# Kernel optimization log

Measured on AMD Instinct MI355X. Metric: run time of the kernel, lower is better.

Reference implementation:

```python
import jax, jax.numpy as jnp
import numpy as np

H = 256

def setup_inputs() -> dict:
    key = jax.random.key(0)
    ks = jax.random.split(key, 9)
    s = 1.0 / np.sqrt(H)
    x = jax.random.normal(ks[0], (8, 2048, H), dtype=jnp.float32)
    Wq = jax.random.uniform(ks[1], (H, H), jnp.float32, -s, s)
    bq = jax.random.uniform(ks[2], (H,), jnp.float32, -s, s)
    Wk = jax.random.uniform(ks[3], (H, H), jnp.float32, -s, s)
    bk = jax.random.uniform(ks[4], (H,), jnp.float32, -s, s)
    Wv = jax.random.uniform(ks[5], (H, H), jnp.float32, -s, s)
    bv = jax.random.uniform(ks[6], (H,), jnp.float32, -s, s)
    Ww = jax.random.uniform(ks[7], (H, 1), jnp.float32, -s, s)
    bw = jax.random.uniform(ks[8], (1,), jnp.float32, -s, s)
    return {"x": x, "Wq": Wq, "bq": bq, "Wk": Wk, "bk": bk,
            "Wv": Wv, "bv": bv, "Ww": Ww, "bw": bw}

def reference(x, Wq, bq, Wk, bk, Wv, bv, Ww, bw):
    # x: (B, N, H) — cross-asset attention over N assets
    q = x @ Wq + bq
    k = x @ Wk + bk
    v = x @ Wv + bv
    scale = 1.0 / jnp.sqrt(jnp.asarray(q.shape[-1], q.dtype))
    beta = jnp.einsum('bnd,bmd->bnm', q, k) * scale  # (B, N, N)
    beta = jax.nn.softmax(beta, axis=-1)
    # original: sum(value[:,None] * beta[...,None], dim=2) == beta @ v
    out = jnp.einsum('bnm,bmd->bnd', beta, v)
    final_scores = (out @ Ww + bw)[..., 0]  # (B, N)
    return final_scores
```

## Files before the change

### kernel.cpp

```cpp
#include <hip/hip_runtime.h>

#define H 256
#define NB 2048
#define BATCH 8
#define NSPLIT 8
#define KSPAN (NB / NSPLIT)

typedef unsigned short u16;
using bf16x8 = __attribute__((ext_vector_type(8))) __bf16;
using f32x4  = __attribute__((ext_vector_type(4))) float;

typedef const __attribute__((address_space(1))) void gv_t;
typedef __attribute__((address_space(3))) void lv_t;

__device__ __forceinline__ void gl_lds16(const void* g, void* l) {
    __builtin_amdgcn_global_load_lds((gv_t*)g, (lv_t*)l, 16, 0, 0);
}

#define MFMA(a, b, c) __builtin_amdgcn_mfma_f32_16x16x32_bf16(a, b, c, 0, 0, 0)

__device__ __forceinline__ u16 f2bf(float f) {
    union { float f; unsigned u; } v; v.f = f;
    unsigned r = v.u + 0x7fffu + ((v.u >> 16) & 1u);
    return (u16)(r >> 16);
}

__global__ __launch_bounds__(256) void prep_kernel(
        const float* __restrict__ Wq, const float* __restrict__ Wk,
        const float* __restrict__ Wv, const float* __restrict__ Ww,
        const float* __restrict__ bq,
        u16* __restrict__ aT, float* __restrict__ wvw, float* __restrict__ kbv) {
    int f = blockIdx.x, t = threadIdx.x;
    __shared__ float wkf[H];
    __shared__ float redp[4], redr[4];
    float wkval = Wk[f * H + t];
    wkf[t] = wkval;
    float p = Wv[f * H + t] * Ww[t];
    float r = wkval * bq[t];
    __syncthreads();
    float s = 0.f;
    #pragma unroll 8
    for (int d = 0; d < H; ++d) s += Wq[t * H + d] * wkf[d];
    aT[f * H + t] = f2bf(s * 0.0625f);
    for (int o = 32; o; o >>= 1) { p += __shfl_xor(p, o); r += __shfl_xor(r, o); }
    int w = t >> 6, lane = t & 63;
    if (lane == 0) { redp[w] = p; redr[w] = r; }
    __syncthreads();
    if (t == 0) {
        wvw[f] = redp[0] + redp[1] + redp[2] + redp[3];
        kbv[f] = redr[0] + redr[1] + redr[2] + redr[3];
    }
}

__global__ __launch_bounds__(256) void cvtu_kernel(
        const float* __restrict__ x, const float* __restrict__ wvw,
        const float* __restrict__ kbv, const float* __restrict__ bv,
        const float* __restrict__ Ww,
        u16* __restrict__ xbf, float* __restrict__ ue, float* __restrict__ ee) {
    int lane = threadIdx.x & 63;
    int row  = blockIdx.x * 4 + (threadIdx.x >> 6);
    float4 xv = *(const float4*)(x + row * H + lane * 4);
    ushort4 o;
    o.x = f2bf(xv.x); o.y = f2bf(xv.y); o.z = f2bf(xv.z); o.w = f2bf(xv.w);
    *(ushort4*)(xbf + row * H + lane * 4) = o;
    float4 wv = *(const float4*)(wvw + lane * 4);
    float s = xv.x * wv.x + xv.y * wv.y + xv.z * wv.z + xv.w * wv.w;
    float4 kv = *(const float4*)(kbv + lane * 4);
    float d = xv.x * kv.x + xv.y * kv.y + xv.z * kv.z + xv.w * kv.w;
    float4 bvv = *(const float4*)(bv + lane * 4);
    float4 www = *(const float4*)(Ww + lane * 4);
    float c = bvv.x * www.x + bvv.y * www.y + bvv.z * www.z + bvv.w * www.w;
    for (int o2 = 32; o2; o2 >>= 1) {
        s += __shfl_xor(s, o2); d += __shfl_xor(d, o2); c += __shfl_xor(c, o2);
    }
    if (lane == 0) {
        float e = __expf(d * 0.0625f);
        ue[row] = e * (s + c);
        ee[row] = e;
    }
}

__global__ __launch_bounds__(256) void projT_kernel(
        const u16* __restrict__ xbf, const u16* __restrict__ aT,
        u16* __restrict__ T) {
    __shared__ u16 bt[16384];
    int tid = threadIdx.x;
    int mb = blockIdx.x * 128, nb = blockIdx.y * 64;
    int w = tid >> 6, lane = tid & 63;
    int l15 = lane & 15, quad = lane >> 4;

    {
        const u16* gsrc = aT + (nb + w * 16 + l15) * H + quad * 8;
        for (int ks = 0; ks < 8; ++ks)
            gl_lds16(gsrc + ks * 32, bt + (w * 8 + ks) * 512);
    }

    bf16x8 a[2][8];
    for (int mi = 0; mi < 2; ++mi) {
        const u16* abase = xbf + (mb + w * 32 + mi * 16 + l15) * H + quad * 8;
        for (int ks = 0; ks < 8; ++ks) a[mi][ks] = *(const bf16x8*)(abase + ks * 32);
    }
    __syncthreads();

    f32x4 acc[2][4] = {};
    for (int ks = 0; ks < 8; ++ks)
        for (int t = 0; t < 4; ++t) {
            bf16x8 b = *(const bf16x8*)(bt + ((t * 8 + ks) * 64 + lane) * 8);
            acc[0][t] = MFMA(a[0][ks], b, acc[0][t]);
            acc[1][t] = MFMA(a[1][ks], b, acc[1][t]);
        }

    for (int mi = 0; mi < 2; ++mi) {
        int m = mb + w * 32 + mi * 16 + quad * 4;
        for (int t = 0; t < 4; ++t) {
            int n = nb + t * 16 + l15;
            for (int r = 0; r < 4; ++r)
                T[(m + r) * H + n] = f2bf(acc[mi][t][r]);
        }
    }
}

__global__ __launch_bounds__(256, 4) void attn_kernel(
        const u16* __restrict__ T, const u16* __restrict__ xbf,
        const float* __restrict__ ue, const float* __restrict__ ee,
        float* __restrict__ pnum, float* __restrict__ pden) {
    __shared__ u16 kt[16384];
    __shared__ float utile[64], etile[64];
    int tid = threadIdx.x;
    int b = blockIdx.y, qb = blockIdx.x * 128, sp = blockIdx.z;
    int w = tid >> 6, lane = tid & 63, l15 = lane & 15, quad = lane >> 4;

    const u16* qb0 = T + (size_t)(b * NB + qb + w * 32 + l15) * H + quad * 8;
    float ls[2][4] = {}, as_[2][4] = {};

    const int kb0 = sp * KSPAN;
    #pragma unroll 1
    for (int kb = kb0; kb < kb0 + KSPAN; kb += 64) {
        const u16* ksrc = xbf + (size_t)(b * NB + kb) * H;
        {
            const u16* gsrc = ksrc + (w * 16 + l15) * H + quad * 8;
            for (int ks = 0; ks < 8; ++ks)
                gl_lds16(gsrc + ks * 32, kt + (w * 8 + ks) * 512);
        }
        if (tid < 64) utile[tid] = ue[b * NB + kb + tid];
        else if (tid < 128) etile[tid - 64] = ee[b * NB + kb + (tid - 64)];
        __syncthreads();

        f32x4 acc[2][4] = {};
        #pragma unroll 1
        for (int half = 0; half < 2; ++half) {
            bf16x8 aq[2][4];
            for (int mi = 0; mi < 2; ++mi)
                for (int kk = 0; kk < 4; ++kk)
                    aq[mi][kk] = *(const bf16x8*)(qb0 + mi * 16 * H + (half * 4 + kk) * 32);
            for (int kk = 0; kk < 4; ++kk) {
                int ks = half * 4 + kk;
                for (int t = 0; t < 4; ++t) {
                    bf16x8 bfr = *(const bf16x8*)(kt + ((t * 8 + ks) * 64 + lane) * 8);
                    acc[0][t] = MFMA(aq[0][kk], bfr, acc[0][t]);
                    acc[1][t] = MFMA(aq[1][kk], bfr, acc[1][t]);
                }
            }
        }

        float uv[4], ev[4];
        for (int t = 0; t < 4; ++t) { uv[t] = utile[t * 16 + l15]; ev[t] = etile[t * 16 + l15]; }

        for (int mi = 0; mi < 2; ++mi)
            for (int r = 0; r < 4; ++r) {
                float p0 = __expf(acc[mi][0][r]), p1 = __expf(acc[mi][1][r]);
                float p2 = __expf(acc[mi][2][r]), p3 = __expf(acc[mi][3][r]);
                ls[mi][r]  += (p0 * ev[0] + p1 * ev[1]) + (p2 * ev[2] + p3 * ev[3]);
                as_[mi][r] += (p0 * uv[0] + p1 * uv[1]) + (p2 * uv[2] + p3 * uv[3]);
            }
        __syncthreads();
    }

    for (int mi = 0; mi < 2; ++mi)
        for (int r = 0; r < 4; ++r)
            for (int o = 1; o < 16; o <<= 1) {
                ls[mi][r]  += __shfl_xor(ls[mi][r], o);
                as_[mi][r] += __shfl_xor(as_[mi][r], o);
            }

    if (l15 == 0) {
        for (int mi = 0; mi < 2; ++mi) {
            size_t base = (size_t)(sp * BATCH + b) * NB + qb + w * 32 + mi * 16 + quad * 4;
            for (int r = 0; r < 4; ++r) {
                pnum[base + r] = as_[mi][r];
                pden[base + r] = ls[mi][r];
            }
        }
    }
}

__global__ __launch_bounds__(256) void finalize_kernel(
        const float* __restrict__ pnum, const float* __restrict__ pden,
        const float* __restrict__ bw, float* __restrict__ out) {
    int i = blockIdx.x * 256 + threadIdx.x;
    float num = 0.f, den = 0.f;
    for (int sp = 0; sp < NSPLIT; ++sp) {
        num += pnum[sp * (BATCH * NB) + i];
        den += pden[sp * (BATCH * NB) + i];
    }
    out[i] = num / den + bw[0];
}

extern "C" void kernel_launch(void* const* d_in, const int* in_sizes, int n_in,
                              void* d_out, int out_size, void* d_ws, size_t ws_size,
                              hipStream_t stream) {
    (void)in_sizes; (void)n_in; (void)out_size; (void)ws_size;
    const float* x  = (const float*)d_in[0];
    const float* Wq = (const float*)d_in[1];
    const float* bq = (const float*)d_in[2];
    const float* Wk = (const float*)d_in[3];
    const float* bk = (const float*)d_in[4];  (void)bk;
    const float* Wv = (const float*)d_in[5];
    const float* bv = (const float*)d_in[6];
    const float* Ww = (const float*)d_in[7];
    const float* bw = (const float*)d_in[8];
    float* out = (float*)d_out;

    u16* xbf = (u16*)d_ws;
    u16* Tbf = xbf + 4194304;
    u16* aT  = Tbf + 4194304;
    float* wvw = (float*)(aT + 65536);
    float* kbv = wvw + 256;
    float* ue  = kbv + 256;
    float* ee  = ue + 16384;
    float* pnum = ee + 16384;
    float* pden = pnum + NSPLIT * BATCH * NB;

    hipLaunchKernelGGL(prep_kernel, dim3(256), dim3(256), 0, stream,
                       Wq, Wk, Wv, Ww, bq, aT, wvw, kbv);
    hipLaunchKernelGGL(cvtu_kernel, dim3(4096), dim3(256), 0, stream,
                       x, wvw, kbv, bv, Ww, xbf, ue, ee);
    hipLaunchKernelGGL(projT_kernel, dim3(128, 4), dim3(256), 0, stream,
                       xbf, aT, Tbf);
    hipLaunchKernelGGL(attn_kernel, dim3(16, 8, NSPLIT), dim3(256), 0, stream,
                       Tbf, xbf, ue, ee, pnum, pden);
    hipLaunchKernelGGL(finalize_kernel, dim3(64), dim3(256), 0, stream,
                       pnum, pden, bw, out);
}
```

Baseline: 148.8 us.

## Double-buffer key tiles in attention and compute Wq·Wk product with MFMA GEMM

The attention kernel now keeps the full Q row fragments in registers and streams 32-key tiles through a double-buffered LDS region, prefetching the next tile while computing the current one. The per-key u/e values are packed into one float2 array read straight from global memory instead of staged in LDS. The weight product aT = Wk·Wqᵀ/16 moves from a scalar loop in prep to the bf16 MFMA GEMM kernel, which is generalised with a scale argument. This adds a kernel launch and rounds Wq/Wk to bf16 before the product, which may reduce accuracy slightly.

```diff
diff --git a/kernel.cpp b/kernel.cpp
--- a/kernel.cpp
+++ b/kernel.cpp
@@ -5,6 +5,7 @@
 #define BATCH 8
 #define NSPLIT 8
 #define KSPAN (NB / NSPLIT)
+#define NHALF (KSPAN / 32)
 
 typedef unsigned short u16;
 using bf16x8 = __attribute__((ext_vector_type(8))) __bf16;
@@ -25,24 +26,21 @@
     return (u16)(r >> 16);
 }
 
-__global__ __launch_bounds__(256) void prep_kernel(
+__global__ __launch_bounds__(256) void wprep_kernel(
         const float* __restrict__ Wq, const float* __restrict__ Wk,
         const float* __restrict__ Wv, const float* __restrict__ Ww,
         const float* __restrict__ bq,
-        u16* __restrict__ aT, float* __restrict__ wvw, float* __restrict__ kbv) {
+        u16* __restrict__ wqb, u16* __restrict__ wkb,
+        float* __restrict__ wvw, float* __restrict__ kbv) {
     int f = blockIdx.x, t = threadIdx.x;
-    __shared__ float wkf[H];
+    float wq = Wq[f * H + t];
+    wqb[f * H + t] = f2bf(wq);
+    float wk = Wk[f * H + t];
+    wkb[f * H + t] = f2bf(wk);
+    float p = Wv[f * H + t] * Ww[t];
+    float r = wk * bq[t];
+    for (int o = 32; o; o >>= 1) { p += __shfl_xor(p, o); r += __shfl_xor(r, o); }
     __shared__ float redp[4], redr[4];
-    float wkval = Wk[f * H + t];
-    wkf[t] = wkval;
-    float p = Wv[f * H + t] * Ww[t];
-    float r = wkval * bq[t];
-    __syncthreads();
-    float s = 0.f;
-    #pragma unroll 8
-    for (int d = 0; d < H; ++d) s += Wq[t * H + d] * wkf[d];
-    aT[f * H + t] = f2bf(s * 0.0625f);
-    for (int o = 32; o; o >>= 1) { p += __shfl_xor(p, o); r += __shfl_xor(r, o); }
     int w = t >> 6, lane = t & 63;
     if (lane == 0) { redp[w] = p; redr[w] = r; }
     __syncthreads();
@@ -56,7 +54,7 @@
         const float* __restrict__ x, const float* __restrict__ wvw,
         const float* __restrict__ kbv, const float* __restrict__ bv,
         const float* __restrict__ Ww,
-        u16* __restrict__ xbf, float* __restrict__ ue, float* __restrict__ ee) {
+        u16* __restrict__ xbf, float2* __restrict__ uee) {
     int lane = threadIdx.x & 63;
     int row  = blockIdx.x * 4 + (threadIdx.x >> 6);
     float4 xv = *(const float4*)(x + row * H + lane * 4);
@@ -75,14 +73,13 @@
     }
     if (lane == 0) {
         float e = __expf(d * 0.0625f);
-        ue[row] = e * (s + c);
-        ee[row] = e;
-    }
-}
-
-__global__ __launch_bounds__(256) void projT_kernel(
-        const u16* __restrict__ xbf, const u16* __restrict__ aT,
-        u16* __restrict__ T) {
+        uee[row] = make_float2(e * (s + c), e);
+    }
+}
+
+__global__ __launch_bounds__(256) void gemm_bt_kernel(
+        const u16* __restrict__ A, const u16* __restrict__ B,
+        u16* __restrict__ C, float scale) {
     __shared__ u16 bt[16384];
     int tid = threadIdx.x;
     int mb = blockIdx.x * 128, nb = blockIdx.y * 64;
@@ -90,14 +87,14 @@
     int l15 = lane & 15, quad = lane >> 4;
 
     {
-        const u16* gsrc = aT + (nb + w * 16 + l15) * H + quad * 8;
+        const u16* gsrc = B + (nb + w * 16 + l15) * H + quad * 8;
         for (int ks = 0; ks < 8; ++ks)
             gl_lds16(gsrc + ks * 32, bt + (w * 8 + ks) * 512);
     }
 
     bf16x8 a[2][8];
     for (int mi = 0; mi < 2; ++mi) {
-        const u16* abase = xbf + (mb + w * 32 + mi * 16 + l15) * H + quad * 8;
+        const u16* abase = A + (size_t)(mb + w * 32 + mi * 16 + l15) * H + quad * 8;
         for (int ks = 0; ks < 8; ++ks) a[mi][ks] = *(const bf16x8*)(abase + ks * 32);
     }
     __syncthreads();
@@ -115,63 +112,75 @@
         for (int t = 0; t < 4; ++t) {
             int n = nb + t * 16 + l15;
             for (int r = 0; r < 4; ++r)
-                T[(m + r) * H + n] = f2bf(acc[mi][t][r]);
+                C[(size_t)(m + r) * H + n] = f2bf(acc[mi][t][r] * scale);
         }
     }
 }
 
 __global__ __launch_bounds__(256, 4) void attn_kernel(
         const u16* __restrict__ T, const u16* __restrict__ xbf,
-        const float* __restrict__ ue, const float* __restrict__ ee,
+        const float2* __restrict__ uee,
         float* __restrict__ pnum, float* __restrict__ pden) {
     __shared__ u16 kt[16384];
-    __shared__ float utile[64], etile[64];
     int tid = threadIdx.x;
     int b = blockIdx.y, qb = blockIdx.x * 128, sp = blockIdx.z;
     int w = tid >> 6, lane = tid & 63, l15 = lane & 15, quad = lane >> 4;
 
-    const u16* qb0 = T + (size_t)(b * NB + qb + w * 32 + l15) * H + quad * 8;
+    bf16x8 aq[2][8];
+    for (int mi = 0; mi < 2; ++mi) {
+        const u16* qbase = T + (size_t)(b * NB + qb + w * 32 + mi * 16 + l15) * H + quad * 8;
+        for (int ks = 0; ks < 8; ++ks) aq[mi][ks] = *(const bf16x8*)(qbase + ks * 32);
+    }
+
+    const u16* xb = xbf + (size_t)b * NB * H;
+    const float2* uep = uee + (size_t)b * NB;
+    const int kb0 = sp * KSPAN;
+
+    int c0 = w * 4;
+    {
+        const u16* g = xb + (size_t)(kb0 + (c0 >> 3) * 16 + l15) * H + (c0 & 7) * 32 + quad * 8;
+        for (int j = 0; j < 4; ++j) {
+            int c = c0 + j;
+            gl_lds16(xb + (size_t)(kb0 + (c >> 3) * 16 + l15) * H + (c & 7) * 32 + quad * 8,
+                     kt + c * 512);
+        }
+        (void)g;
+    }
+    __syncthreads();
+
     float ls[2][4] = {}, as_[2][4] = {};
 
-    const int kb0 = sp * KSPAN;
     #pragma unroll 1
-    for (int kb = kb0; kb < kb0 + KSPAN; kb += 64) {
-        const u16* ksrc = xbf + (size_t)(b * NB + kb) * H;
-        {
-            const u16* gsrc = ksrc + (w * 16 + l15) * H + quad * 8;
-            for (int ks = 0; ks < 8; ++ks)
-                gl_lds16(gsrc + ks * 32, kt + (w * 8 + ks) * 512);
-        }
-        if (tid < 64) utile[tid] = ue[b * NB + kb + tid];
-        else if (tid < 128) etile[tid - 64] = ee[b * NB + kb + (tid - 64)];
-        __syncthreads();
-
-        f32x4 acc[2][4] = {};
-        #pragma unroll 1
-        for (int half = 0; half < 2; ++half) {
-            bf16x8 aq[2][4];
-            for (int mi = 0; mi < 2; ++mi)
-                for (int kk = 0; kk < 4; ++kk)
-                    aq[mi][kk] = *(const bf16x8*)(qb0 + mi * 16 * H + (half * 4 + kk) * 32);
-            for (int kk = 0; kk < 4; ++kk) {
-                int ks = half * 4 + kk;
-                for (int t = 0; t < 4; ++t) {
-                    bf16x8 bfr = *(const bf16x8*)(kt + ((t * 8 + ks) * 64 + lane) * 8);
-                    acc[0][t] = MFMA(aq[0][kk], bfr, acc[0][t]);
-                    acc[1][t] = MFMA(aq[1][kk], bfr, acc[1][t]);
-                }
-            }
-        }
-
-        float uv[4], ev[4];
-        for (int t = 0; t < 4; ++t) { uv[t] = utile[t * 16 + l15]; ev[t] = etile[t * 16 + l15]; }
+    for (int h = 0; h < NHALF; ++h) {
+        int cur = h & 1;
+        if (h + 1 < NHALF) {
+            int kb32 = kb0 + (h + 1) * 32;
+            u16* dst = kt + (cur ^ 1) * 8192;
+            for (int j = 0; j < 4; ++j) {
+                int c = c0 + j;
+                gl_lds16(xb + (size_t)(kb32 + (c >> 3) * 16 + l15) * H + (c & 7) * 32 + quad * 8,
+                         dst + c * 512);
+            }
+        }
+        int kb32 = kb0 + h * 32;
+        float2 ue0 = uep[kb32 + l15];
+        float2 ue1 = uep[kb32 + 16 + l15];
+
+        const u16* ktc = kt + cur * 8192;
+        f32x4 acc[2][2] = {};
+        for (int ks = 0; ks < 8; ++ks)
+            for (int t = 0; t < 2; ++t) {
+                bf16x8 bfr = *(const bf16x8*)(ktc + ((t * 8 + ks) * 64 + lane) * 8);
+                acc[0][t] = MFMA(aq[0][ks], bfr, acc[0][t]);
+                acc[1][t] = MFMA(aq[1][ks], bfr, acc[1][t]);
+            }
 
         for (int mi = 0; mi < 2; ++mi)
             for (int r = 0; r < 4; ++r) {
-                float p0 = __expf(acc[mi][0][r]), p1 = __expf(acc[mi][1][r]);
-                float p2 = __expf(acc[mi][2][r]), p3 = __expf(acc[mi][3][r]);
-                ls[mi][r]  += (p0 * ev[0] + p1 * ev[1]) + (p2 * ev[2] + p3 * ev[3]);
-                as_[mi][r] += (p0 * uv[0] + p1 * uv[1]) + (p2 * uv[2] + p3 * uv[3]);
+                float p0 = __expf(acc[mi][0][r]);
+                float p1 = __expf(acc[mi][1][r]);
+                as_[mi][r] += p0 * ue0.x + p1 * ue1.x;
+                ls[mi][r]  += p0 * ue0.y + p1 * ue1.y;
             }
         __syncthreads();
     }
@@ -223,22 +232,25 @@
 
     u16* xbf = (u16*)d_ws;
     u16* Tbf = xbf + 4194304;
-    u16* aT  = Tbf + 4194304;
-    float* wvw = (float*)(aT + 65536);
+    u16* aTb = Tbf + 4194304;
+    u16* wqb = aTb + 65536;
+    u16* wkb = wqb + 65536;
+    float* wvw = (float*)(wkb + 65536);
     float* kbv = wvw + 256;
-    float* ue  = kbv + 256;
-    float* ee  = ue + 16384;
-    float* pnum = ee + 16384;
+    float2* uee = (float2*)(kbv + 256);
+    float* pnum = (float*)(uee + 16384);
     float* pden = pnum + NSPLIT * BATCH * NB;
 
-    hipLaunchKernelGGL(prep_kernel, dim3(256), dim3(256), 0, stream,
-                       Wq, Wk, Wv, Ww, bq, aT, wvw, kbv);
+    hipLaunchKernelGGL(wprep_kernel, dim3(256), dim3(256), 0, stream,
+                       Wq, Wk, Wv, Ww, bq, wqb, wkb, wvw, kbv);
+    hipLaunchKernelGGL(gemm_bt_kernel, dim3(2, 4), dim3(256), 0, stream,
+                       wkb, wqb, aTb, 0.0625f);
     hipLaunchKernelGGL(cvtu_kernel, dim3(4096), dim3(256), 0, stream,
-                       x, wvw, kbv, bv, Ww, xbf, ue, ee);
-    hipLaunchKernelGGL(projT_kernel, dim3(128, 4), dim3(256), 0, stream,
-                       xbf, aT, Tbf);
+                       x, wvw, kbv, bv, Ww, xbf, uee);
+    hipLaunchKernelGGL(gemm_bt_kernel, dim3(128, 4), dim3(256), 0, stream,
+                       xbf, aTb, Tbf, 1.0f);
     hipLaunchKernelGGL(attn_kernel, dim3(16, 8, NSPLIT), dim3(256), 0, stream,
-                       Tbf, xbf, ue, ee, pnum, pden);
+                       Tbf, xbf, uee, pnum, pden);
     hipLaunchKernelGGL(finalize_kernel, dim3(64), dim3(256), 0, stream,
                        pnum, pden, bw, out);
 }
```

Result: faster. 129.1 us (-13.3%).
